# Kernel tuning notes

Measured on AMD Instinct MI355X. Metric: run time of the kernel, lower is better.

## Reference

```python
import jax, jax.numpy as jnp
from jax import lax
import numpy as np

B, OBS, PRED, F, H = 2048, 20, 30, 16, 1024


def _lstm_layer(x, Wih, Whh, bih, bhh):
    # x: [T, B, in]; PyTorch gate order i, f, g, o; zero initial state
    Bb = x.shape[1]
    Hh = Whh.shape[1]
    def step(carry, xt):
        h, c = carry
        g = xt @ Wih.T + h @ Whh.T + bih + bhh
        i, f, gg, o = jnp.split(g, 4, axis=-1)
        c = jax.nn.sigmoid(f) * c + jax.nn.sigmoid(i) * jnp.tanh(gg)
        h = jax.nn.sigmoid(o) * jnp.tanh(c)
        return (h, c), h
    z = jnp.zeros((Bb, Hh), x.dtype)
    _, hs = lax.scan(step, (z, z), x)
    return hs  # [T, B, H]


def _lstm2(x, Wih0, Whh0, bih0, bhh0, Wih1, Whh1, bih1, bhh1):
    return _lstm_layer(_lstm_layer(x, Wih0, Whh0, bih0, bhh0), Wih1, Whh1, bih1, bhh1)


def setup_inputs() -> dict:
    key = jax.random.key(0)
    ks = jax.random.split(key, 32)
    s = 0.05
    def w(k, shape):
        return jax.random.normal(k, shape, dtype=jnp.float32) * s
    d = {
        'x_in': jax.random.normal(ks[0], (B, OBS, F), dtype=jnp.float32),
        'y': jax.random.normal(ks[1], (B, PRED, F), dtype=jnp.float32),
        'v_in': jax.random.normal(ks[2], (B, OBS, F), dtype=jnp.float32),
        'sx': jnp.ones((1,), jnp.float32),
        'sv': jnp.ones((1,), jnp.float32),
    }
    i = 3
    for p in ['v', 'a']:
        d[p + 'Wih0'] = w(ks[i], (4 * H, F)); i += 1
        d[p + 'Whh0'] = w(ks[i], (4 * H, H)); i += 1
        d[p + 'bih0'] = w(ks[i], (4 * H,)); i += 1
        d[p + 'bhh0'] = w(ks[i], (4 * H,)); i += 1
        d[p + 'Wih1'] = w(ks[i], (4 * H, H)); i += 1
        d[p + 'Whh1'] = w(ks[i], (4 * H, H)); i += 1
        d[p + 'bih1'] = w(ks[i], (4 * H,)); i += 1
        d[p + 'bhh1'] = w(ks[i], (4 * H,)); i += 1
        d[p + 'Wl'] = w(ks[i], (F, H)); i += 1
        d[p + 'bl'] = w(ks[i], (F,)); i += 1
    return d


def reference(x_in, y, v_in, sx, sv,
              vWih0, vWhh0, vbih0, vbhh0, vWih1, vWhh1, vbih1, vbhh1, vWl, vbl,
              aWih0, aWhh0, abih0, abhh0, aWih1, aWhh1, abih1, abhh1, aWl, abl):
    # last observed position, scaled: [1, B, F]
    x = jnp.transpose(x_in, (1, 0, 2))[-1:] * sx
    yT = sx * jnp.transpose(y, (1, 0, 2))  # [PRED, B, F]
    v_seq = jnp.transpose(v_in, (1, 0, 2))  # [OBS, B, F]
    a_seq = v_seq[1:] - v_seq[:-1]          # [OBS-1, B, F]

    vh = _lstm2(v_seq, vWih0, vWhh0, vbih0, vbhh0, vWih1, vWhh1, vbih1, vbhh1)
    v = sv * jnp.tanh(vh[-1:] @ vWl.T + vbl)  # [1, B, F]

    ah = _lstm2(a_seq, aWih0, aWhh0, abih0, abhh0, aWih1, aWhh1, abih1, abhh1)
    a = jnp.tanh(ah @ aWl.T + abl)[-1:]       # [1, B, F] (unscaled, fed back)

    v = v + sv * a
    x = x + v

    def body(carry, _):
        a, v, x = carry
        # NOTE: faithful to source -- LSTM state resets to zero each step
        ah = _lstm2(a, aWih0, aWhh0, abih0, abhh0, aWih1, aWhh1, abih1, abhh1)
        a = jnp.tanh(ah @ aWl.T + abl)
        v = v + sv * a
        x = x + v
        return (a, v, x), x[0]

    _, xs = lax.scan(body, (a, v, x), None, length=PRED - 1)  # xs: [PRED-1, B, F]
    out = jnp.concatenate([x, xs], axis=0)  # [PRED, B, F]
    return (out, yT)
```

## Files before the change

### kernel.cpp

```cpp
#include <hip/hip_runtime.h>


#define B_    2048
#define OBS_  20
#define PRED_ 30
#define F_    16
#define H_    1024
#define GN_   4096

typedef _Float16 f16;
typedef _Float16 f16x8 __attribute__((ext_vector_type(8)));
typedef _Float16 f16x4 __attribute__((ext_vector_type(4)));
typedef float    f32x4 __attribute__((ext_vector_type(4)));

__device__ __forceinline__ float fast_sigmoid(float x) {
  return 1.0f / (1.0f + __expf(-x));
}
__device__ __forceinline__ float fast_tanh(float x) {
  float ax = fabsf(x);
  float e  = __expf(-2.0f * ax);
  float r  = (1.0f - e) / (1.0f + e);
  return copysignf(r, x);
}

template<int K16, int NMAIN, int HASC, int WRITEC>
__global__ __launch_bounds__(256, 2)
void lstm_step(const f16* __restrict__ A16, const f16* __restrict__ W16,
               const f16* __restrict__ A0,  const f16* __restrict__ W0,
               const f16* __restrict__ A1,  const f16* __restrict__ W1,
               const float* __restrict__ bias,
               const float* __restrict__ cin, float* __restrict__ cout,
               f16* __restrict__ hout)
{
  __shared__ f16 lA[2][128 * 64];
  __shared__ f16 lB[2][128 * 64];

  const int tid  = threadIdx.x;
  const int lane = tid & 63;
  const int wv   = tid >> 6;
  const int wr   = wv >> 1;
  const int wc   = wv & 1;
  const int bm   = blockIdx.x >> 5;
  const int bn   = blockIdx.x & 31;
  const int b0   = bm * 128;
  const int j0   = bn * 32;

  const int lcol = lane & 15;
  const int lkq  = lane >> 4;
  const int jcol = j0 + wc * 16 + lcol;

  f32x4 acc[4][4];
#pragma unroll
  for (int g = 0; g < 4; ++g) {
    float bv = bias[g * H_ + jcol];
#pragma unroll
    for (int m = 0; m < 4; ++m) acc[m][g] = (f32x4){bv, bv, bv, bv};
  }

  auto stageA = [&](int buf, const f16* Asrc, int k0) {
#pragma unroll
    for (int cc = 0; cc < 4; ++cc) {
      int o  = cc * 4096 + tid * 16;
      int rr = o >> 7;
      int sp = (o >> 4) & 7;
      int sl = sp ^ (rr & 7);
      const f16* gp = Asrc + (b0 + rr) * H_ + k0 + sl * 8;
      __builtin_amdgcn_global_load_lds(
          (const __attribute__((address_space(1))) void*)gp,
          (__attribute__((address_space(3))) void*)((char*)&lA[buf][0] + o),
          16, 0, 0);
    }
  };
  auto stageB = [&](int buf, const f16* Wsrc, int k0) {
#pragma unroll
    for (int cc = 0; cc < 4; ++cc) {
      int o  = cc * 4096 + tid * 16;
      int rr = o >> 7;
      int sp = (o >> 4) & 7;
      int sl = sp ^ (rr & 7);
      int row = (rr >> 5) * H_ + j0 + (rr & 31);
      const f16* gp = Wsrc + row * H_ + k0 + sl * 8;
      __builtin_amdgcn_global_load_lds(
          (const __attribute__((address_space(1))) void*)gp,
          (__attribute__((address_space(3))) void*)((char*)&lB[buf][0] + o),
          16, 0, 0);
    }
  };

  if (NMAIN > 0) { stageA(0, A0, 0); stageB(0, W0, 0); }

  if (K16) {
    f16x8 za = {0, 0, 0, 0, 0, 0, 0, 0};
    f16x8 af[4], bf[4];
#pragma unroll
    for (int m = 0; m < 4; ++m) {
      if (lkq < 2) {
        int row = b0 + wr * 64 + m * 16 + lcol;
        af[m] = *(const f16x8*)(A16 + row * 16 + lkq * 8);
      } else af[m] = za;
    }
#pragma unroll
    for (int g = 0; g < 4; ++g) {
      if (lkq < 2) {
        int row = g * H_ + j0 + wc * 16 + lcol;
        bf[g] = *(const f16x8*)(W16 + row * 16 + lkq * 8);
      } else bf[g] = za;
    }
#pragma unroll
    for (int m = 0; m < 4; ++m)
#pragma unroll
      for (int g = 0; g < 4; ++g)
        acc[m][g] = __builtin_amdgcn_mfma_f32_16x16x32_f16(af[m], bf[g], acc[m][g], 0, 0, 0);
  }

  if (NMAIN > 0) {
    const int NT = NMAIN * 16;
    __syncthreads();
    int cur = 0;
    for (int t = 0; t < NT; ++t) {
      if (t + 1 < NT) {
        int tn = t + 1;
        const f16* As = (NMAIN == 2 && tn >= 16) ? A1 : A0;
        const f16* Ws = (NMAIN == 2 && tn >= 16) ? W1 : W0;
        int k0 = (tn & 15) * 64;
        stageA(cur ^ 1, As, k0);
        stageB(cur ^ 1, Ws, k0);
      }
#pragma unroll
      for (int ks = 0; ks < 2; ++ks) {
        f16x8 av[4], bv_[4];
#pragma unroll
        for (int m = 0; m < 4; ++m) {
          int ar = wr * 64 + m * 16 + lcol;
          int sl = (ks * 4 + lkq) ^ (ar & 7);
          av[m] = *(const f16x8*)&lA[cur][ar * 64 + sl * 8];
        }
#pragma unroll
        for (int g = 0; g < 4; ++g) {
          int br = g * 32 + wc * 16 + lcol;
          int sl = (ks * 4 + lkq) ^ (br & 7);
          bv_[g] = *(const f16x8*)&lB[cur][br * 64 + sl * 8];
        }
#pragma unroll
        for (int m = 0; m < 4; ++m)
#pragma unroll
          for (int g = 0; g < 4; ++g)
            acc[m][g] = __builtin_amdgcn_mfma_f32_16x16x32_f16(av[m], bv_[g], acc[m][g], 0, 0, 0);
      }
      __syncthreads();
      cur ^= 1;
    }
  }

#pragma unroll
  for (int m = 0; m < 4; ++m) {
    int brow0 = b0 + wr * 64 + m * 16 + lkq * 4;
#pragma unroll
    for (int r = 0; r < 4; ++r) {
      int bi = (brow0 + r) * H_ + jcol;
      float gi = acc[m][0][r];
      float gf = acc[m][1][r];
      float gg = acc[m][2][r];
      float go = acc[m][3][r];
      float cold = HASC ? cin[bi] : 0.0f;
      float cn = fast_sigmoid(gf) * cold + fast_sigmoid(gi) * fast_tanh(gg);
      float hv = fast_sigmoid(go) * fast_tanh(cn);
      if (WRITEC) cout[bi] = cn;
      hout[bi] = (f16)hv;
    }
  }
}

template<int MODE>
__global__ __launch_bounds__(256)
void proj_update(const f16* __restrict__ h1, const float* __restrict__ Wl,
                 const float* __restrict__ bl, const float* __restrict__ sv,
                 float* __restrict__ v_buf, float* __restrict__ x_buf,
                 float* __restrict__ out_t, f16* __restrict__ a16)
{
  __shared__ f16 lh[16 * 1024];
  const int b0r = blockIdx.x * 16;
  const int tid = threadIdx.x;
#pragma unroll
  for (int c = 0; c < 8; ++c) {
    int o = c * 256 + tid;
    *(f16x8*)&lh[o * 8] = *(const f16x8*)&h1[b0r * 1024 + o * 8];
  }
  __syncthreads();
  const int br = tid >> 4;
  const int f  = tid & 15;
  float s0 = 0, s1 = 0, s2 = 0, s3 = 0;
  const float4* wp = (const float4*)(Wl + f * 1024);
#pragma unroll 4
  for (int k8 = 0; k8 < 128; ++k8) {
    f16x8 hv = *(const f16x8*)&lh[br * 1024 + k8 * 8];
    float4 w0 = wp[k8 * 2], w1 = wp[k8 * 2 + 1];
    s0 += (float)hv[0] * w0.x + (float)hv[4] * w1.x;
    s1 += (float)hv[1] * w0.y + (float)hv[5] * w1.y;
    s2 += (float)hv[2] * w0.z + (float)hv[6] * w1.z;
    s3 += (float)hv[3] * w0.w + (float)hv[7] * w1.w;
  }
  float t = fast_tanh(bl[f] + ((s0 + s1) + (s2 + s3)));
  int idx = (b0r + br) * F_ + f;
  if (MODE == 0) {
    v_buf[idx] = sv[0] * t;
  } else {
    float v = v_buf[idx] + sv[0] * t;
    v_buf[idx] = v;
    float x = x_buf[idx] + v;
    x_buf[idx] = x;
    out_t[idx] = x;
    a16[idx] = (f16)t;
  }
}

__global__ void prep_kernel(const float* __restrict__ x_in, const float* __restrict__ y,
                            const float* __restrict__ v_in, const float* __restrict__ sx,
                            float* __restrict__ out, float* __restrict__ x_buf,
                            f16* __restrict__ xt16, f16* __restrict__ at16)
{
  const float s = sx[0];
  int gid = blockIdx.x * blockDim.x + threadIdx.x;
  int gs  = gridDim.x * blockDim.x;
  for (int i = gid; i < B_ * OBS_ * F_; i += gs) {
    int b = i / (OBS_ * F_);
    int rem = i - b * (OBS_ * F_);
    int t = rem >> 4;
    int f = rem & 15;
    float v = v_in[i];
    xt16[(t * B_ + b) * F_ + f] = (f16)v;
    if (t < OBS_ - 1) {
      float v2 = v_in[i + F_];
      at16[(t * B_ + b) * F_ + f] = (f16)(v2 - v);
    }
  }
  for (int i = gid; i < PRED_ * B_ * F_; i += gs) {
    int t = i / (B_ * F_);
    int rem = i - t * (B_ * F_);
    int b = rem >> 4;
    int f = rem & 15;
    out[PRED_ * B_ * F_ + i] = s * y[(b * PRED_ + t) * F_ + f];
  }
  for (int i = gid; i < B_ * F_; i += gs) {
    int b = i >> 4;
    int f = i & 15;
    x_buf[i] = s * x_in[(b * OBS_ + (OBS_ - 1)) * F_ + f];
  }
}

struct ConvArgs {
  const float* src[8];
  f16*         dst[8];
  int          n[8];
  const float* b1[4];
  const float* b2[4];
  float*       bd[4];
};

__global__ void convw(ConvArgs a)
{
  int gid = blockIdx.x * blockDim.x + threadIdx.x;
  int gs  = gridDim.x * blockDim.x;
#pragma unroll
  for (int s = 0; s < 8; ++s) {
    int n4 = a.n[s] >> 2;
    for (int i = gid; i < n4; i += gs) {
      float4 v = ((const float4*)a.src[s])[i];
      f16x4 d = {(f16)v.x, (f16)v.y, (f16)v.z, (f16)v.w};
      ((f16x4*)a.dst[s])[i] = d;
    }
  }
#pragma unroll
  for (int s = 0; s < 4; ++s) {
    for (int i = gid; i < GN_; i += gs) a.bd[s][i] = a.b1[s][i] + a.b2[s][i];
  }
}

extern "C" void kernel_launch(void* const* d_in, const int* in_sizes, int n_in,
                              void* d_out, int out_size, void* d_ws, size_t ws_size,
                              hipStream_t stream)
{
  (void)in_sizes; (void)n_in; (void)out_size; (void)ws_size;

  const float* x_in  = (const float*)d_in[0];
  const float* y     = (const float*)d_in[1];
  const float* v_in  = (const float*)d_in[2];
  const float* sx    = (const float*)d_in[3];
  const float* sv    = (const float*)d_in[4];
  const float* vWih0 = (const float*)d_in[5];
  const float* vWhh0 = (const float*)d_in[6];
  const float* vbih0 = (const float*)d_in[7];
  const float* vbhh0 = (const float*)d_in[8];
  const float* vWih1 = (const float*)d_in[9];
  const float* vWhh1 = (const float*)d_in[10];
  const float* vbih1 = (const float*)d_in[11];
  const float* vbhh1 = (const float*)d_in[12];
  const float* vWl   = (const float*)d_in[13];
  const float* vbl   = (const float*)d_in[14];
  const float* aWih0 = (const float*)d_in[15];
  const float* aWhh0 = (const float*)d_in[16];
  const float* abih0 = (const float*)d_in[17];
  const float* abhh0 = (const float*)d_in[18];
  const float* aWih1 = (const float*)d_in[19];
  const float* aWhh1 = (const float*)d_in[20];
  const float* abih1 = (const float*)d_in[21];
  const float* abhh1 = (const float*)d_in[22];
  const float* aWl   = (const float*)d_in[23];
  const float* abl   = (const float*)d_in[24];
  float* out = (float*)d_out;

  char* ws = (char*)d_ws;
  size_t off = 0;
  auto alloc = [&](size_t bytes) {
    char* p = ws + off;
    off += (bytes + 255) & ~(size_t)255;
    return p;
  };
  f16* vWih0f = (f16*)alloc((size_t)GN_ * F_ * 2);
  f16* vWhh0f = (f16*)alloc((size_t)GN_ * H_ * 2);
  f16* vWih1f = (f16*)alloc((size_t)GN_ * H_ * 2);
  f16* vWhh1f = (f16*)alloc((size_t)GN_ * H_ * 2);
  f16* aWih0f = (f16*)alloc((size_t)GN_ * F_ * 2);
  f16* aWhh0f = (f16*)alloc((size_t)GN_ * H_ * 2);
  f16* aWih1f = (f16*)alloc((size_t)GN_ * H_ * 2);
  f16* aWhh1f = (f16*)alloc((size_t)GN_ * H_ * 2);
  float* vb0 = (float*)alloc(GN_ * 4);
  float* vb1 = (float*)alloc(GN_ * 4);
  float* ab0 = (float*)alloc(GN_ * 4);
  float* ab1 = (float*)alloc(GN_ * 4);
  f16* xt16 = (f16*)alloc((size_t)OBS_ * B_ * F_ * 2);
  f16* at16 = (f16*)alloc((size_t)(OBS_ - 1) * B_ * F_ * 2);
  f16* h0a = (f16*)alloc((size_t)B_ * H_ * 2);
  f16* h0b = (f16*)alloc((size_t)B_ * H_ * 2);
  f16* h1a = (f16*)alloc((size_t)B_ * H_ * 2);
  f16* h1b = (f16*)alloc((size_t)B_ * H_ * 2);
  float* c0 = (float*)alloc((size_t)B_ * H_ * 4);
  float* c1 = (float*)alloc((size_t)B_ * H_ * 4);
  f16* a16   = (f16*)alloc((size_t)B_ * F_ * 2);
  float* v_buf = (float*)alloc((size_t)B_ * F_ * 4);
  float* x_buf = (float*)alloc((size_t)B_ * F_ * 4);

  ConvArgs ca;
  ca.src[0] = vWih0; ca.dst[0] = vWih0f; ca.n[0] = GN_ * F_;
  ca.src[1] = vWhh0; ca.dst[1] = vWhh0f; ca.n[1] = GN_ * H_;
  ca.src[2] = vWih1; ca.dst[2] = vWih1f; ca.n[2] = GN_ * H_;
  ca.src[3] = vWhh1; ca.dst[3] = vWhh1f; ca.n[3] = GN_ * H_;
  ca.src[4] = aWih0; ca.dst[4] = aWih0f; ca.n[4] = GN_ * F_;
  ca.src[5] = aWhh0; ca.dst[5] = aWhh0f; ca.n[5] = GN_ * H_;
  ca.src[6] = aWih1; ca.dst[6] = aWih1f; ca.n[6] = GN_ * H_;
  ca.src[7] = aWhh1; ca.dst[7] = aWhh1f; ca.n[7] = GN_ * H_;
  ca.b1[0] = vbih0; ca.b2[0] = vbhh0; ca.bd[0] = vb0;
  ca.b1[1] = vbih1; ca.b2[1] = vbhh1; ca.bd[1] = vb1;
  ca.b1[2] = abih0; ca.b2[2] = abhh0; ca.bd[2] = ab0;
  ca.b1[3] = abih1; ca.b2[3] = abhh1; ca.bd[3] = ab1;
  convw<<<1024, 256, 0, stream>>>(ca);
  prep_kernel<<<1024, 256, 0, stream>>>(x_in, y, v_in, sx, out, x_buf, xt16, at16);

  dim3 gG(512), gB(256);

  const f16 *h0p = nullptr, *h1p = nullptr;
  for (int t = 0; t < OBS_; ++t) {
    f16* h0o = (t & 1) ? h0b : h0a;
    f16* h1o = (t & 1) ? h1b : h1a;
    if (t == 0) {
      lstm_step<1, 0, 0, 1><<<gG, gB, 0, stream>>>(xt16 + (size_t)t * B_ * F_, vWih0f,
          nullptr, nullptr, nullptr, nullptr, vb0, nullptr, c0, h0o);
      lstm_step<0, 1, 0, 1><<<gG, gB, 0, stream>>>(nullptr, nullptr, h0o, vWih1f,
          nullptr, nullptr, vb1, nullptr, c1, h1o);
    } else {
      lstm_step<1, 1, 1, 1><<<gG, gB, 0, stream>>>(xt16 + (size_t)t * B_ * F_, vWih0f,
          h0p, vWhh0f, nullptr, nullptr, vb0, c0, c0, h0o);
      lstm_step<0, 2, 1, 1><<<gG, gB, 0, stream>>>(nullptr, nullptr, h0o, vWih1f,
          h1p, vWhh1f, vb1, c1, c1, h1o);
    }
    h0p = h0o; h1p = h1o;
  }
  proj_update<0><<<128, 256, 0, stream>>>(h1p, vWl, vbl, sv, v_buf, nullptr, nullptr, nullptr);

  h0p = nullptr; h1p = nullptr;
  for (int t = 0; t < OBS_ - 1; ++t) {
    f16* h0o = (t & 1) ? h0b : h0a;
    f16* h1o = (t & 1) ? h1b : h1a;
    if (t == 0) {
      lstm_step<1, 0, 0, 1><<<gG, gB, 0, stream>>>(at16 + (size_t)t * B_ * F_, aWih0f,
          nullptr, nullptr, nullptr, nullptr, ab0, nullptr, c0, h0o);
      lstm_step<0, 1, 0, 1><<<gG, gB, 0, stream>>>(nullptr, nullptr, h0o, aWih1f,
          nullptr, nullptr, ab1, nullptr, c1, h1o);
    } else {
      lstm_step<1, 1, 1, 1><<<gG, gB, 0, stream>>>(at16 + (size_t)t * B_ * F_, aWih0f,
          h0p, aWhh0f, nullptr, nullptr, ab0, c0, c0, h0o);
      lstm_step<0, 2, 1, 1><<<gG, gB, 0, stream>>>(nullptr, nullptr, h0o, aWih1f,
          h1p, aWhh1f, ab1, c1, c1, h1o);
    }
    h0p = h0o; h1p = h1o;
  }
  proj_update<1><<<128, 256, 0, stream>>>(h1p, aWl, abl, sv, v_buf, x_buf, out, a16);

  for (int t = 1; t < PRED_; ++t) {
    lstm_step<1, 0, 0, 0><<<gG, gB, 0, stream>>>(a16, aWih0f,
        nullptr, nullptr, nullptr, nullptr, ab0, nullptr, nullptr, h0a);
    lstm_step<0, 1, 0, 0><<<gG, gB, 0, stream>>>(nullptr, nullptr, h0a, aWih1f,
        nullptr, nullptr, ab1, nullptr, nullptr, h1a);
    proj_update<1><<<128, 256, 0, stream>>>(h1a, aWl, abl, sv, v_buf, x_buf,
        out + (size_t)t * B_ * F_, a16);
  }
}
```

Baseline: 4.934 ms.

## Batch v/a LSTM stacks into one grid and fuse prediction scan into persistent kernel

The v and a LSTM stacks now run concurrently: each step launches 1024 blocks, where the upper half of the batch rows use the a-weights on the acceleration inputs, halving the number of recurrent launches over the observation window. The 29-step prediction loop becomes one persistent kernel that uses atomic grid barriers between layer0, layer1 and the projection, replacing many small launches. The K tile is reduced to 32 with half the LDS, allowing 4 blocks per CU. This risks barrier overhead, and if the 512 blocks are not all co-resident the persistent kernel can deadlock.

Result: slower. 9.268 ms (+87.8%).

```diff
diff --git a/kernel.cpp b/kernel.cpp
--- a/kernel.cpp
+++ b/kernel.cpp
@@ -23,151 +23,249 @@
   return copysignf(r, x);
 }
 
-template<int K16, int NMAIN, int HASC, int WRITEC>
-__global__ __launch_bounds__(256, 2)
-void lstm_step(const f16* __restrict__ A16, const f16* __restrict__ W16,
-               const f16* __restrict__ A0,  const f16* __restrict__ W0,
-               const f16* __restrict__ A1,  const f16* __restrict__ W1,
-               const float* __restrict__ bias,
-               const float* __restrict__ cin, float* __restrict__ cout,
-               f16* __restrict__ hout)
-{
-  __shared__ f16 lA[2][128 * 64];
-  __shared__ f16 lB[2][128 * 64];
-
-  const int tid  = threadIdx.x;
-  const int lane = tid & 63;
-  const int wv   = tid >> 6;
-  const int wr   = wv >> 1;
-  const int wc   = wv & 1;
-  const int bm   = blockIdx.x >> 5;
-  const int bn   = blockIdx.x & 31;
-  const int b0   = bm * 128;
-  const int j0   = bn * 32;
-
-  const int lcol = lane & 15;
-  const int lkq  = lane >> 4;
-  const int jcol = j0 + wc * 16 + lcol;
-
-  f32x4 acc[4][4];
+__device__ __forceinline__ void stageA(f16* dst, const f16* Asrc, int b0, int k0, int tid) {
+#pragma unroll
+  for (int cc = 0; cc < 2; ++cc) {
+    int o  = cc * 4096 + tid * 16;
+    int rr = o >> 6;
+    int sp = (o >> 4) & 3;
+    int sl = sp ^ ((rr >> 1) & 3);
+    const f16* gp = Asrc + (size_t)(b0 + rr) * H_ + k0 + sl * 8;
+    __builtin_amdgcn_global_load_lds(
+        (const __attribute__((address_space(1))) void*)gp,
+        (__attribute__((address_space(3))) void*)((char*)dst + o), 16, 0, 0);
+  }
+}
+__device__ __forceinline__ void stageB(f16* dst, const f16* Wsrc, int j0, int k0, int tid) {
+#pragma unroll
+  for (int cc = 0; cc < 2; ++cc) {
+    int o  = cc * 4096 + tid * 16;
+    int rr = o >> 6;
+    int sp = (o >> 4) & 3;
+    int sl = sp ^ ((rr >> 1) & 3);
+    int row = (rr >> 5) * H_ + j0 + (rr & 31);
+    const f16* gp = Wsrc + (size_t)row * H_ + k0 + sl * 8;
+    __builtin_amdgcn_global_load_lds(
+        (const __attribute__((address_space(1))) void*)gp,
+        (__attribute__((address_space(3))) void*)((char*)dst + o), 16, 0, 0);
+  }
+}
+
+__device__ __forceinline__ void acc_init(f32x4 (&acc)[4][4], const float* bias, int jcol) {
 #pragma unroll
   for (int g = 0; g < 4; ++g) {
     float bv = bias[g * H_ + jcol];
 #pragma unroll
     for (int m = 0; m < 4; ++m) acc[m][g] = (f32x4){bv, bv, bv, bv};
   }
-
-  auto stageA = [&](int buf, const f16* Asrc, int k0) {
-#pragma unroll
-    for (int cc = 0; cc < 4; ++cc) {
-      int o  = cc * 4096 + tid * 16;
-      int rr = o >> 7;
-      int sp = (o >> 4) & 7;
-      int sl = sp ^ (rr & 7);
-      const f16* gp = Asrc + (b0 + rr) * H_ + k0 + sl * 8;
-      __builtin_amdgcn_global_load_lds(
-          (const __attribute__((address_space(1))) void*)gp,
-          (__attribute__((address_space(3))) void*)((char*)&lA[buf][0] + o),
-          16, 0, 0);
-    }
-  };
-  auto stageB = [&](int buf, const f16* Wsrc, int k0) {
-#pragma unroll
-    for (int cc = 0; cc < 4; ++cc) {
-      int o  = cc * 4096 + tid * 16;
-      int rr = o >> 7;
-      int sp = (o >> 4) & 7;
-      int sl = sp ^ (rr & 7);
-      int row = (rr >> 5) * H_ + j0 + (rr & 31);
-      const f16* gp = Wsrc + row * H_ + k0 + sl * 8;
-      __builtin_amdgcn_global_load_lds(
-          (const __attribute__((address_space(1))) void*)gp,
-          (__attribute__((address_space(3))) void*)((char*)&lB[buf][0] + o),
-          16, 0, 0);
-    }
-  };
-
-  if (NMAIN > 0) { stageA(0, A0, 0); stageB(0, W0, 0); }
-
-  if (K16) {
-    f16x8 za = {0, 0, 0, 0, 0, 0, 0, 0};
-    f16x8 af[4], bf[4];
+}
+
+__device__ __forceinline__ void run_k16(f32x4 (&acc)[4][4], const f16* A16, const f16* W16,
+    int b0, int j0, int wr, int wc, int lcol, int lkq)
+{
+  f16x8 za = {0, 0, 0, 0, 0, 0, 0, 0};
+  f16x8 af[4], bf[4];
+#pragma unroll
+  for (int m = 0; m < 4; ++m) {
+    if (lkq < 2) {
+      int row = b0 + wr * 64 + m * 16 + lcol;
+      af[m] = *(const f16x8*)(A16 + (size_t)row * 16 + lkq * 8);
+    } else af[m] = za;
+  }
+#pragma unroll
+  for (int g = 0; g < 4; ++g) {
+    if (lkq < 2) {
+      int row = g * H_ + j0 + wc * 16 + lcol;
+      bf[g] = *(const f16x8*)(W16 + (size_t)row * 16 + lkq * 8);
+    } else bf[g] = za;
+  }
+#pragma unroll
+  for (int m = 0; m < 4; ++m)
+#pragma unroll
+    for (int g = 0; g < 4; ++g)
+      acc[m][g] = __builtin_amdgcn_mfma_f32_16x16x32_f16(af[m], bf[g], acc[m][g], 0, 0, 0);
+}
+
+template<int NMAIN>
+__device__ __forceinline__ void run_kloop(f32x4 (&acc)[4][4], f16 (*lA)[4096], f16 (*lB)[4096],
+    const f16* A0, const f16* W0, const f16* A1, const f16* W1,
+    int b0, int j0, int tid, int wr, int wc, int lcol, int lkq)
+{
+  const int NT = NMAIN * 32;
+  __syncthreads();
+  int cur = 0;
+  for (int t = 0; t < NT; ++t) {
+    if (t + 1 < NT) {
+      int tn = t + 1;
+      const f16* As = (NMAIN == 2 && tn >= 32) ? A1 : A0;
+      const f16* Ws = (NMAIN == 2 && tn >= 32) ? W1 : W0;
+      int k0 = (tn & 31) * 32;
+      stageA(lA[cur ^ 1], As, b0, k0, tid);
+      stageB(lB[cur ^ 1], Ws, j0, k0, tid);
+    }
+    f16x8 av[4], bw[4];
 #pragma unroll
     for (int m = 0; m < 4; ++m) {
-      if (lkq < 2) {
-        int row = b0 + wr * 64 + m * 16 + lcol;
-        af[m] = *(const f16x8*)(A16 + row * 16 + lkq * 8);
-      } else af[m] = za;
+      int ar = wr * 64 + m * 16 + lcol;
+      int sa = lkq ^ ((ar >> 1) & 3);
+      av[m] = *(const f16x8*)&lA[cur][ar * 32 + sa * 8];
     }
 #pragma unroll
     for (int g = 0; g < 4; ++g) {
-      if (lkq < 2) {
-        int row = g * H_ + j0 + wc * 16 + lcol;
-        bf[g] = *(const f16x8*)(W16 + row * 16 + lkq * 8);
-      } else bf[g] = za;
+      int br = g * 32 + wc * 16 + lcol;
+      int sb = lkq ^ ((br >> 1) & 3);
+      bw[g] = *(const f16x8*)&lB[cur][br * 32 + sb * 8];
     }
 #pragma unroll
     for (int m = 0; m < 4; ++m)
 #pragma unroll
       for (int g = 0; g < 4; ++g)
-        acc[m][g] = __builtin_amdgcn_mfma_f32_16x16x32_f16(af[m], bf[g], acc[m][g], 0, 0, 0);
-  }
-
-  if (NMAIN > 0) {
-    const int NT = NMAIN * 16;
+        acc[m][g] = __builtin_amdgcn_mfma_f32_16x16x32_f16(av[m], bw[g], acc[m][g], 0, 0, 0);
     __syncthreads();
-    int cur = 0;
-    for (int t = 0; t < NT; ++t) {
-      if (t + 1 < NT) {
-        int tn = t + 1;
-        const f16* As = (NMAIN == 2 && tn >= 16) ? A1 : A0;
-        const f16* Ws = (NMAIN == 2 && tn >= 16) ? W1 : W0;
-        int k0 = (tn & 15) * 64;
-        stageA(cur ^ 1, As, k0);
-        stageB(cur ^ 1, Ws, k0);
-      }
-#pragma unroll
-      for (int ks = 0; ks < 2; ++ks) {
-        f16x8 av[4], bv_[4];
-#pragma unroll
-        for (int m = 0; m < 4; ++m) {
-          int ar = wr * 64 + m * 16 + lcol;
-          int sl = (ks * 4 + lkq) ^ (ar & 7);
-          av[m] = *(const f16x8*)&lA[cur][ar * 64 + sl * 8];
-        }
-#pragma unroll
-        for (int g = 0; g < 4; ++g) {
-          int br = g * 32 + wc * 16 + lcol;
-          int sl = (ks * 4 + lkq) ^ (br & 7);
-          bv_[g] = *(const f16x8*)&lB[cur][br * 64 + sl * 8];
-        }
-#pragma unroll
-        for (int m = 0; m < 4; ++m)
-#pragma unroll
-          for (int g = 0; g < 4; ++g)
-            acc[m][g] = __builtin_amdgcn_mfma_f32_16x16x32_f16(av[m], bv_[g], acc[m][g], 0, 0, 0);
-      }
-      __syncthreads();
-      cur ^= 1;
-    }
-  }
-
+    cur ^= 1;
+  }
+}
+
+__device__ __forceinline__ void lstm_epi(f32x4 (&acc)[4][4], const float* cin, float* cout,
+    f16* hout, int b0, int jcol, int wr, int lkq, bool hasc, bool writec)
+{
 #pragma unroll
   for (int m = 0; m < 4; ++m) {
     int brow0 = b0 + wr * 64 + m * 16 + lkq * 4;
 #pragma unroll
     for (int r = 0; r < 4; ++r) {
-      int bi = (brow0 + r) * H_ + jcol;
-      float gi = acc[m][0][r];
-      float gf = acc[m][1][r];
-      float gg = acc[m][2][r];
-      float go = acc[m][3][r];
-      float cold = HASC ? cin[bi] : 0.0f;
+      size_t bi = (size_t)(brow0 + r) * H_ + jcol;
+      float gi = acc[m][0][r], gf = acc[m][1][r], gg = acc[m][2][r], go = acc[m][3][r];
+      float cold = hasc ? cin[bi] : 0.0f;
       float cn = fast_sigmoid(gf) * cold + fast_sigmoid(gi) * fast_tanh(gg);
       float hv = fast_sigmoid(go) * fast_tanh(cn);
-      if (WRITEC) cout[bi] = cn;
+      if (writec) cout[bi] = cn;
       hout[bi] = (f16)hv;
     }
+  }
+}
+
+struct StepArgs {
+  const f16* A16;
+  const f16* W16v; const f16* W16a;
+  const f16* A0;  const f16* W0v; const f16* W0a;
+  const f16* A1;  const f16* W1v; const f16* W1a;
+  const float* bv; const float* ba;
+  const float* cin; float* cout; f16* hout;
+};
+
+template<int K16, int NMAIN, int HASC, int WRITEC>
+__global__ __launch_bounds__(256, 4)
+void lstm_step(StepArgs p)
+{
+  __shared__ f16 lA[2][4096];
+  __shared__ f16 lB[2][4096];
+  const int tid = threadIdx.x, lane = tid & 63;
+  const int wv = tid >> 6, wr = wv >> 1, wc = wv & 1;
+  const int bm = blockIdx.x >> 5, bn = blockIdx.x & 31;
+  const int b0 = bm * 128, j0 = bn * 32;
+  const int ch = bm >> 4;
+  const int lcol = lane & 15, lkq = lane >> 4;
+  const int jcol = j0 + wc * 16 + lcol;
+
+  const f16* W16 = ch ? p.W16a : p.W16v;
+  const f16* W0  = ch ? p.W0a  : p.W0v;
+  const f16* W1  = ch ? p.W1a  : p.W1v;
+  const float* bias = ch ? p.ba : p.bv;
+
+  if (NMAIN > 0) { stageA(lA[0], p.A0, b0, 0, tid); stageB(lB[0], W0, j0, 0, tid); }
+
+  f32x4 acc[4][4];
+  acc_init(acc, bias, jcol);
+  if (K16) run_k16(acc, p.A16, W16, b0, j0, wr, wc, lcol, lkq);
+  if (NMAIN > 0)
+    run_kloop<NMAIN>(acc, lA, lB, p.A0, W0, p.A1, W1, b0, j0, tid, wr, wc, lcol, lkq);
+  lstm_epi(acc, p.cin, p.cout, p.hout, b0, jcol, wr, lkq, HASC != 0, WRITEC != 0);
+}
+
+__device__ __forceinline__ void grid_bar(unsigned* bar, unsigned target) {
+  __syncthreads();
+  if (threadIdx.x == 0) {
+    __hip_atomic_fetch_add(bar, 1u, __ATOMIC_ACQ_REL, __HIP_MEMORY_SCOPE_AGENT);
+    while (__hip_atomic_load(bar, __ATOMIC_ACQUIRE, __HIP_MEMORY_SCOPE_AGENT) < target) {
+      __builtin_amdgcn_s_sleep(2);
+    }
+  }
+  __syncthreads();
+}
+
+struct ScanArgs {
+  const f16 *Wih0, *Wih1;
+  const float *b0g, *b1g;
+  const float *Wl, *bl, *sv;
+  f16 *a16; float *v_buf, *x_buf; float *out;
+  f16 *h0, *h1;
+  unsigned *bar;
+};
+
+__global__ __launch_bounds__(256, 4)
+void scan_kernel(ScanArgs s)
+{
+  __shared__ f16 lA[2][4096];
+  __shared__ f16 lB[2][4096];
+  const int tid = threadIdx.x, lane = tid & 63;
+  const int wv = tid >> 6, wr = wv >> 1, wc = wv & 1;
+  const int bm = blockIdx.x >> 5, bn = blockIdx.x & 31;
+  const int b0 = bm * 128, j0 = bn * 32;
+  const int lcol = lane & 15, lkq = lane >> 4;
+  const int jcol = j0 + wc * 16 + lcol;
+  unsigned tgt = 0;
+
+  for (int t = 1; t < PRED_; ++t) {
+    {
+      f32x4 acc[4][4];
+      acc_init(acc, s.b0g, jcol);
+      run_k16(acc, s.a16, s.Wih0, b0, j0, wr, wc, lcol, lkq);
+      lstm_epi(acc, nullptr, nullptr, s.h0, b0, jcol, wr, lkq, false, false);
+    }
+    tgt += 512; grid_bar(s.bar, tgt);
+
+    {
+      f32x4 acc[4][4];
+      acc_init(acc, s.b1g, jcol);
+      stageA(lA[0], s.h0, b0, 0, tid);
+      stageB(lB[0], s.Wih1, j0, 0, tid);
+      run_kloop<1>(acc, lA, lB, s.h0, s.Wih1, nullptr, nullptr, b0, j0, tid, wr, wc, lcol, lkq);
+      lstm_epi(acc, nullptr, nullptr, s.h1, b0, jcol, wr, lkq, false, false);
+    }
+    tgt += 512; grid_bar(s.bar, tgt);
+
+    {
+      int d = tid >> 2, q = tid & 3;
+      int row = blockIdx.x * 4 + (d >> 4), f = d & 15;
+      const f16* hp = s.h1 + (size_t)row * H_ + q * 256;
+      const float* wp = s.Wl + (size_t)f * H_ + q * 256;
+      float a0 = 0, a1 = 0, a2 = 0, a3 = 0;
+#pragma unroll 8
+      for (int i = 0; i < 256; i += 8) {
+        f16x8 h8 = *(const f16x8*)(hp + i);
+        float4 w0 = *(const float4*)(wp + i);
+        float4 w1 = *(const float4*)(wp + i + 4);
+        a0 += (float)h8[0] * w0.x + (float)h8[4] * w1.x;
+        a1 += (float)h8[1] * w0.y + (float)h8[5] * w1.y;
+        a2 += (float)h8[2] * w0.z + (float)h8[6] * w1.z;
+        a3 += (float)h8[3] * w0.w + (float)h8[7] * w1.w;
+      }
+      float acc = (a0 + a1) + (a2 + a3);
+      acc += __shfl_down(acc, 1);
+      acc += __shfl_down(acc, 2);
+      if (q == 0) {
+        float tv = fast_tanh(acc + s.bl[f]);
+        int idx = row * F_ + f;
+        float v = s.v_buf[idx] + s.sv[0] * tv;
+        s.v_buf[idx] = v;
+        float x = s.x_buf[idx] + v;
+        s.x_buf[idx] = x;
+        s.out[(size_t)t * B_ * F_ + idx] = x;
+        s.a16[idx] = (f16)tv;
+      }
+    }
+    if (t < PRED_ - 1) { tgt += 512; grid_bar(s.bar, tgt); }
   }
 }
 
@@ -184,13 +282,13 @@
 #pragma unroll
   for (int c = 0; c < 8; ++c) {
     int o = c * 256 + tid;
-    *(f16x8*)&lh[o * 8] = *(const f16x8*)&h1[b0r * 1024 + o * 8];
+    *(f16x8*)&lh[o * 8] = *(const f16x8*)&h1[(size_t)b0r * 1024 + o * 8];
   }
   __syncthreads();
   const int br = tid >> 4;
   const int f  = tid & 15;
   float s0 = 0, s1 = 0, s2 = 0, s3 = 0;
-  const float4* wp = (const float4*)(Wl + f * 1024);
+  const float4* wp = (const float4*)(Wl + (size_t)f * 1024);
 #pragma unroll 4
   for (int k8 = 0; k8 < 128; ++k8) {
     f16x8 hv = *(const f16x8*)&lh[br * 1024 + k8 * 8];
@@ -217,7 +315,7 @@
 __global__ void prep_kernel(const float* __restrict__ x_in, const float* __restrict__ y,
                             const float* __restrict__ v_in, const float* __restrict__ sx,
                             float* __restrict__ out, float* __restrict__ x_buf,
-                            f16* __restrict__ xt16, f16* __restrict__ at16)
+                            f16* __restrict__ m16)
 {
   const float s = sx[0];
   int gid = blockIdx.x * blockDim.x + threadIdx.x;
@@ -228,11 +326,9 @@
     int t = rem >> 4;
     int f = rem & 15;
     float v = v_in[i];
-    xt16[(t * B_ + b) * F_ + f] = (f16)v;
-    if (t < OBS_ - 1) {
-      float v2 = v_in[i + F_];
-      at16[(t * B_ + b) * F_ + f] = (f16)(v2 - v);
-    }
+    m16[((size_t)t * 4096 + b) * F_ + f] = (f16)v;
+    if (t < OBS_ - 1)
+      m16[((size_t)t * 4096 + 2048 + b) * F_ + f] = (f16)(v_in[i + F_] - v);
   }
   for (int i = gid; i < PRED_ * B_ * F_; i += gs) {
     int t = i / (B_ * F_);
@@ -328,17 +424,19 @@
   float* vb1 = (float*)alloc(GN_ * 4);
   float* ab0 = (float*)alloc(GN_ * 4);
   float* ab1 = (float*)alloc(GN_ * 4);
-  f16* xt16 = (f16*)alloc((size_t)OBS_ * B_ * F_ * 2);
-  f16* at16 = (f16*)alloc((size_t)(OBS_ - 1) * B_ * F_ * 2);
-  f16* h0a = (f16*)alloc((size_t)B_ * H_ * 2);
-  f16* h0b = (f16*)alloc((size_t)B_ * H_ * 2);
-  f16* h1a = (f16*)alloc((size_t)B_ * H_ * 2);
-  f16* h1b = (f16*)alloc((size_t)B_ * H_ * 2);
-  float* c0 = (float*)alloc((size_t)B_ * H_ * 4);
-  float* c1 = (float*)alloc((size_t)B_ * H_ * 4);
+  f16* m16 = (f16*)alloc((size_t)OBS_ * 4096 * F_ * 2);
+  f16* h0a = (f16*)alloc((size_t)4096 * H_ * 2);
+  f16* h0b = (f16*)alloc((size_t)4096 * H_ * 2);
+  f16* h1a = (f16*)alloc((size_t)4096 * H_ * 2);
+  f16* h1b = (f16*)alloc((size_t)4096 * H_ * 2);
+  float* c0 = (float*)alloc((size_t)4096 * H_ * 4);
+  float* c1 = (float*)alloc((size_t)4096 * H_ * 4);
   f16* a16   = (f16*)alloc((size_t)B_ * F_ * 2);
   float* v_buf = (float*)alloc((size_t)B_ * F_ * 4);
   float* x_buf = (float*)alloc((size_t)B_ * F_ * 4);
+  unsigned* bar = (unsigned*)alloc(256);
+
+  hipMemsetAsync(bar, 0, 256, stream);
 
   ConvArgs ca;
   ca.src[0] = vWih0; ca.dst[0] = vWih0f; ca.n[0] = GN_ * F_;
@@ -354,54 +452,48 @@
   ca.b1[2] = abih0; ca.b2[2] = abhh0; ca.bd[2] = ab0;
   ca.b1[3] = abih1; ca.b2[3] = abhh1; ca.bd[3] = ab1;
   convw<<<1024, 256, 0, stream>>>(ca);
-  prep_kernel<<<1024, 256, 0, stream>>>(x_in, y, v_in, sx, out, x_buf, xt16, at16);
-
-  dim3 gG(512), gB(256);
-
-  const f16 *h0p = nullptr, *h1p = nullptr;
+  prep_kernel<<<1024, 256, 0, stream>>>(x_in, y, v_in, sx, out, x_buf, m16);
+
+  f16 *h0cur = h0a, *h1cur = h1a;
+  const f16 *h0prev = nullptr, *h1prev = nullptr;
   for (int t = 0; t < OBS_; ++t) {
-    f16* h0o = (t & 1) ? h0b : h0a;
-    f16* h1o = (t & 1) ? h1b : h1a;
+    int grid = (t < OBS_ - 1) ? 1024 : 512;
+    h0cur = (t & 1) ? h0b : h0a;
+    h1cur = (t & 1) ? h1b : h1a;
+
+    StepArgs q{};
+    q.A16 = m16 + (size_t)t * 4096 * F_;
+    q.W16v = vWih0f; q.W16a = aWih0f;
+    q.bv = vb0; q.ba = ab0;
+    q.cout = c0; q.hout = h0cur;
     if (t == 0) {
-      lstm_step<1, 0, 0, 1><<<gG, gB, 0, stream>>>(xt16 + (size_t)t * B_ * F_, vWih0f,
-          nullptr, nullptr, nullptr, nullptr, vb0, nullptr, c0, h0o);
-      lstm_step<0, 1, 0, 1><<<gG, gB, 0, stream>>>(nullptr, nullptr, h0o, vWih1f,
-          nullptr, nullptr, vb1, nullptr, c1, h1o);
+      lstm_step<1, 0, 0, 1><<<grid, 256, 0, stream>>>(q);
     } else {
-      lstm_step<1, 1, 1, 1><<<gG, gB, 0, stream>>>(xt16 + (size_t)t * B_ * F_, vWih0f,
-          h0p, vWhh0f, nullptr, nullptr, vb0, c0, c0, h0o);
-      lstm_step<0, 2, 1, 1><<<gG, gB, 0, stream>>>(nullptr, nullptr, h0o, vWih1f,
-          h1p, vWhh1f, vb1, c1, c1, h1o);
-    }
-    h0p = h0o; h1p = h1o;
-  }
-  proj_update<0><<<128, 256, 0, stream>>>(h1p, vWl, vbl, sv, v_buf, nullptr, nullptr, nullptr);
-
-  h0p = nullptr; h1p = nullptr;
-  for (int t = 0; t < OBS_ - 1; ++t) {
-    f16* h0o = (t & 1) ? h0b : h0a;
-    f16* h1o = (t & 1) ? h1b : h1a;
+      q.A0 = h0prev; q.W0v = vWhh0f; q.W0a = aWhh0f; q.cin = c0;
+      lstm_step<1, 1, 1, 1><<<grid, 256, 0, stream>>>(q);
+    }
+
+    StepArgs r{};
+    r.A0 = h0cur; r.W0v = vWih1f; r.W0a = aWih1f;
+    r.bv = vb1; r.ba = ab1;
+    r.cout = c1; r.hout = h1cur;
     if (t == 0) {
-      lstm_step<1, 0, 0, 1><<<gG, gB, 0, stream>>>(at16 + (size_t)t * B_ * F_, aWih0f,
-          nullptr, nullptr, nullptr, nullptr, ab0, nullptr, c0, h0o);
-      lstm_step<0, 1, 0, 1><<<gG, gB, 0, stream>>>(nullptr, nullptr, h0o, aWih1f,
-          nullptr, nullptr, ab1, nullptr, c1, h1o);
+      lstm_step<0, 1, 0, 1><<<grid, 256, 0, stream>>>(r);
     } else {
-      lstm_step<1, 1, 1, 1><<<gG, gB, 0, stream>>>(at16 + (size_t)t * B_ * F_, aWih0f,
-          h0p, aWhh0f, nullptr, nullptr, ab0, c0, c0, h0o);
-      lstm_step<0, 2, 1, 1><<<gG, gB, 0, stream>>>(nullptr, nullptr, h0o, aWih1f,
-          h1p, aWhh1f, ab1, c1, c1, h1o);
-    }
-    h0p = h0o; h1p = h1o;
-  }
-  proj_update<1><<<128, 256, 0, stream>>>(h1p, aWl, abl, sv, v_buf, x_buf, out, a16);
-
-  for (int t = 1; t < PRED_; ++t) {
-    lstm_step<1, 0, 0, 0><<<gG, gB, 0, stream>>>(a16, aWih0f,
-        nullptr, nullptr, nullptr, nullptr, ab0, nullptr, nullptr, h0a);
-    lstm_step<0, 1, 0, 0><<<gG, gB, 0, stream>>>(nullptr, nullptr, h0a, aWih1f,
-        nullptr, nullptr, ab1, nullptr, nullptr, h1a);
-    proj_update<1><<<128, 256, 0, stream>>>(h1a, aWl, abl, sv, v_buf, x_buf,
-        out + (size_t)t * B_ * F_, a16);
-  }
-}
+      r.A1 = h1prev; r.W1v = vWhh1f; r.W1a = aWhh1f; r.cin = c1;
+      lstm_step<0, 2, 1, 1><<<grid, 256, 0, stream>>>(r);
+    }
+    h0prev = h0cur; h1prev = h1cur;
+  }
+
+  proj_update<0><<<128, 256, 0, stream>>>(h1cur, vWl, vbl, sv, v_buf, nullptr, nullptr, nullptr);
+  proj_update<1><<<128, 256, 0, stream>>>(h1a + (size_t)2048 * H_, aWl, abl, sv,
+                                          v_buf, x_buf, out, a16);
+
+  ScanArgs sa{};
+  sa.Wih0 = aWih0f; sa.Wih1 = aWih1f; sa.b0g = ab0; sa.b1g = ab1;
+  sa.Wl = aWl; sa.bl = abl; sa.sv = sv;
+  sa.a16 = a16; sa.v_buf = v_buf; sa.x_buf = x_buf; sa.out = out;
+  sa.h0 = h0a; sa.h1 = h1a; sa.bar = bar;
+  scan_kernel<<<512, 256, 0, stream>>>(sa);
+}
```
